# Optimization experiments

Measured on AMD Instinct MI355X. Metric: run time of the kernel, lower is better.

Reference implementation:

```python
import jax, jax.numpy as jnp
import numpy as np

B, S, H = 2, 2048, 1024
N, DK = 16, 64          # heads, key/value dim (N*DK == H)
DF = 4096               # FFN hidden
SCALE = 1.0 / float(DK) ** 0.5
EPS = 1e-5


def _layer_norm(x, g, b):
    mu = jnp.mean(x, axis=-1, keepdims=True)
    var = jnp.var(x, axis=-1, keepdims=True)
    return (x - mu) * jax.lax.rsqrt(var + EPS) * g + b


def setup_inputs() -> dict:
    key = jax.random.key(0)
    ks = jax.random.split(key, 12)
    s = 0.02
    return {
        "x": jax.random.normal(ks[0], (B, S, H), dtype=jnp.float32),
        "Wq": jax.random.normal(ks[1], (N * DK, H), dtype=jnp.float32) * s,
        "bq": jnp.zeros((N * DK,), jnp.float32),
        "Wk": jax.random.normal(ks[2], (N * DK, H), dtype=jnp.float32) * s,
        "bk": jnp.zeros((N * DK,), jnp.float32),
        "Wv": jax.random.normal(ks[3], (N * DK, H), dtype=jnp.float32) * s,
        "bv": jnp.zeros((N * DK,), jnp.float32),
        "Wo": jax.random.normal(ks[4], (H, N * DK), dtype=jnp.float32) * s,
        "bo": jnp.zeros((H,), jnp.float32),
        "W1": jax.random.normal(ks[5], (DF, H), dtype=jnp.float32) * s,
        "b1": jnp.zeros((DF,), jnp.float32),
        "W2": jax.random.normal(ks[6], (H, DF), dtype=jnp.float32) * s,
        "b2": jnp.zeros((H,), jnp.float32),
        "ln1_g": jnp.ones((H,), jnp.float32),
        "ln1_b": jnp.zeros((H,), jnp.float32),
        "ln2_g": jnp.ones((H,), jnp.float32),
        "ln2_b": jnp.zeros((H,), jnp.float32),
    }


def _mha(x, Wq, bq, Wk, bk, Wv, bv, Wo, bo):
    b = x.shape[0]
    q = (x @ Wq.T + bq).reshape(b, -1, N, DK)  # [B,T,N,DK]
    k = (x @ Wk.T + bk).reshape(b, -1, N, DK)
    v = (x @ Wv.T + bv).reshape(b, -1, N, DK)
    # naive full-score attention, faithful to torch einsum layout
    scores = jnp.einsum('btnd,bsnd->tsbn', q, k) * SCALE  # [T,S,B,N]
    p = jax.nn.softmax(scores, axis=1)                    # softmax over S (dim=1)
    attn = jnp.einsum('tsbn,bsnd->btnd', p, v)            # [B,T,N,DK]
    attn = attn.reshape(b, attn.shape[1], -1)             # [B,T,N*DK]
    return attn @ Wo.T + bo


def reference(x, Wq, bq, Wk, bk, Wv, bv, Wo, bo, W1, b1, W2, b2,
              ln1_g, ln1_b, ln2_g, ln2_b):
    # post-LN encoder layer: x = LN(x + MHA(x)); x = LN(x + FFN(x))
    h = _layer_norm(x + _mha(x, Wq, bq, Wk, bk, Wv, bv, Wo, bo), ln1_g, ln1_b)
    ff = jax.nn.relu(h @ W1.T + b1) @ W2.T + b2
    return _layer_norm(h + ff, ln2_g, ln2_b)
```

## Files before the change

### kernel.cpp

```cpp
#include <hip/hip_runtime.h>
#include <stdint.h>


typedef unsigned short u16;
typedef __bf16 bf16x8 __attribute__((ext_vector_type(8)));
typedef float  f32x4  __attribute__((ext_vector_type(4)));

__device__ __forceinline__ u16 f2bf(float f) {
    unsigned int u = __float_as_uint(f);
    u += 0x7FFFu + ((u >> 16) & 1u);
    return (u16)(u >> 16);
}

__device__ __forceinline__ float bf2f(u16 v) {
    return __uint_as_float((unsigned)v << 16);
}

__device__ __forceinline__ unsigned pack_bf16_hi(float lo, float hi) {
#if __has_builtin(__builtin_amdgcn_perm)
    return __builtin_amdgcn_perm(__float_as_uint(hi), __float_as_uint(lo), 0x07060302u);
#else
    return (__float_as_uint(lo) >> 16) | (__float_as_uint(hi) & 0xFFFF0000u);
#endif
}

__device__ __forceinline__ void async_load16(const u16* g, u16* l) {
    __builtin_amdgcn_global_load_lds(
        (__attribute__((address_space(1))) void*)g,
        (__attribute__((address_space(3))) void*)l, 16, 0, 0);
}

struct CvtArgs {
    const float* src[7];
    u16*         dst[7];
    int          n[7];
};

__global__ __launch_bounds__(256) void k_cvt_all(CvtArgs a) {
    const int seg = blockIdx.y;
    const int i = (blockIdx.x * 256 + threadIdx.x) * 8;
    if (i >= a.n[seg]) return;
    const float* in = a.src[seg];
    u16* out = a.dst[seg];
    float4 x = *(const float4*)(in + i);
    float4 y = *(const float4*)(in + i + 4);
    uint4 o;
    o.x = (unsigned)f2bf(x.x) | ((unsigned)f2bf(x.y) << 16);
    o.y = (unsigned)f2bf(x.z) | ((unsigned)f2bf(x.w) << 16);
    o.z = (unsigned)f2bf(y.x) | ((unsigned)f2bf(y.y) << 16);
    o.w = (unsigned)f2bf(y.z) | ((unsigned)f2bf(y.w) << 16);
    *(uint4*)(out + i) = o;
}

__global__ __launch_bounds__(256) void k_concat3(const float* __restrict__ a,
                                                 const float* __restrict__ b,
                                                 const float* __restrict__ c,
                                                 float* __restrict__ out) {
    int i = blockIdx.x * 256 + threadIdx.x;
    if (i >= 3072) return;
    out[i] = (i < 1024) ? a[i] : (i < 2048 ? b[i - 1024] : c[i - 2048]);
}

template<int OUT_BF16, int RELU>
__global__ __launch_bounds__(512, 2) void k_gemm256(
    const u16* __restrict__ A, const u16* __restrict__ Bw,
    const float* __restrict__ bias, void* __restrict__ Y,
    int M, int N, int K)
{
    __shared__ u16 As[2][256 * 64];
    __shared__ u16 Bs[2][256 * 64];
    const int tid  = threadIdx.x;
    const int wave = tid >> 6, lane = tid & 63;
    const int lm = lane & 15, lq = lane >> 4;
    const int wr = wave >> 2;
    const int wc = wave & 3;
    const int m0 = blockIdx.x * 256, n0 = blockIdx.y * 256;
    const int ksz = K / gridDim.z;
    const int ks  = blockIdx.z * ksz;
    const int NT  = ksz >> 6;

    size_t goffA[4], goffB[4];
#pragma unroll
    for (int i = 0; i < 4; i++) {
        const int c = i * 512 + tid;
        const int row = c >> 3, kcp = c & 7;
        const int kcl = kcp ^ (row & 7);
        goffA[i] = (size_t)(m0 + row) * K + kcl * 8;
        goffB[i] = (size_t)(n0 + row) * K + kcl * 8;
    }

    const int ach0 = ((0 + lq) ^ (lm & 7)) * 8;
    const int ach1 = ((4 + lq) ^ (lm & 7)) * 8;
    const int albase = (wr * 128 + lm) * 64;
    const int blbase = (wc * 64 + lm) * 64;

    f32x4 acc[8][4];
#pragma unroll
    for (int i = 0; i < 8; i++)
#pragma unroll
        for (int j = 0; j < 4; j++) acc[i][j] = (f32x4){0.f, 0.f, 0.f, 0.f};

#define STAGE256(T, p)                                                          \
    {                                                                           \
        const int k0_ = ks + (T) * 64;                                          \
        _Pragma("unroll")                                                       \
        for (int i_ = 0; i_ < 4; i_++) {                                        \
            async_load16(A  + goffA[i_] + k0_,                                  \
                         &As[p][(i_ * 512 + wave * 64) * 8]);                   \
            async_load16(Bw + goffB[i_] + k0_,                                  \
                         &Bs[p][(i_ * 512 + wave * 64) * 8]);                   \
        }                                                                       \
    }

#define LOADQ(dst, q)                                                           \
    {                                                                           \
        _Pragma("unroll")                                                       \
        for (int ii_ = 0; ii_ < 2; ii_++) {                                     \
            dst[ii_][0] = *(const bf16x8*)(Ab + albase + ((q)*2 + ii_) * 1024 + ach0); \
            dst[ii_][1] = *(const bf16x8*)(Ab + albase + ((q)*2 + ii_) * 1024 + ach1); \
        }                                                                       \
    }

#define MFMAQ(src, q)                                                           \
    {                                                                           \
        _Pragma("unroll")                                                       \
        for (int ii_ = 0; ii_ < 2; ii_++)                                       \
            _Pragma("unroll")                                                   \
            for (int j_ = 0; j_ < 4; j_++) {                                    \
                acc[(q)*2 + ii_][j_] = __builtin_amdgcn_mfma_f32_16x16x32_bf16( \
                    src[ii_][0], bfr[0][j_], acc[(q)*2 + ii_][j_], 0, 0, 0);    \
                acc[(q)*2 + ii_][j_] = __builtin_amdgcn_mfma_f32_16x16x32_bf16( \
                    src[ii_][1], bfr[1][j_], acc[(q)*2 + ii_][j_], 0, 0, 0);    \
            }                                                                   \
    }

    STAGE256(0, 0);
    STAGE256(1, 1);
    asm volatile("s_waitcnt vmcnt(8)" ::: "memory");
    __builtin_amdgcn_s_barrier();
    __builtin_amdgcn_sched_barrier(0);

    for (int T = 0; T < NT; ++T) {
        const int p = T & 1;
        const u16* Ab = As[p];
        const u16* Bb = Bs[p];

        bf16x8 bfr[2][4];
#pragma unroll
        for (int j = 0; j < 4; j++) {
            bfr[0][j] = *(const bf16x8*)(Bb + blbase + j * 1024 + ach0);
            bfr[1][j] = *(const bf16x8*)(Bb + blbase + j * 1024 + ach1);
        }
        bf16x8 aA[2][2], aB[2][2];
        LOADQ(aA, 0);
        LOADQ(aB, 1);
        MFMAQ(aA, 0);
        LOADQ(aA, 2);
        MFMAQ(aB, 1);
        LOADQ(aB, 3);
        MFMAQ(aA, 2);
        MFMAQ(aB, 3);

        __builtin_amdgcn_sched_barrier(0);
        __builtin_amdgcn_s_barrier();
        __builtin_amdgcn_sched_barrier(0);

        if (T + 2 < NT) {
            STAGE256(T + 2, p);
            asm volatile("s_waitcnt vmcnt(8)" ::: "memory");
            __builtin_amdgcn_s_barrier();
            __builtin_amdgcn_sched_barrier(0);
        } else if (T + 1 < NT) {
            asm volatile("s_waitcnt vmcnt(0)" ::: "memory");
            __builtin_amdgcn_s_barrier();
            __builtin_amdgcn_sched_barrier(0);
        }
    }
#undef STAGE256
#undef LOADQ
#undef MFMAQ

    const float bsc = (blockIdx.z == 0) ? 1.f : 0.f;
    const size_t zoff = (size_t)blockIdx.z * M * N;
#pragma unroll
    for (int i = 0; i < 8; i++) {
        const int mg = m0 + wr * 128 + i * 16 + lq * 4;
#pragma unroll
        for (int j = 0; j < 4; j++) {
            const int ng = n0 + wc * 64 + j * 16 + lm;
            const float bv = bias[ng] * bsc;
#pragma unroll
            for (int r = 0; r < 4; r++) {
                float v = acc[i][j][r] + bv;
                if (RELU) v = fmaxf(v, 0.f);
                if (OUT_BF16) ((u16*)Y)[zoff + (size_t)(mg + r) * N + ng] = f2bf(v);
                else          ((float*)Y)[zoff + (size_t)(mg + r) * N + ng] = v;
            }
        }
    }
}

template<int OUT_BF16, int RELU>
__global__ __launch_bounds__(256, 4) void k_gemm_bt(
    const u16* __restrict__ A, const u16* __restrict__ Bw,
    const float* __restrict__ bias, void* __restrict__ Y,
    int M, int N, int K)
{
    __shared__ u16 As[128 * 64];
    __shared__ u16 Bs[128 * 64];
    const int tid  = threadIdx.x;
    const int wave = tid >> 6, lane = tid & 63;
    const int lm = lane & 15, lq = lane >> 4;
    const int m0 = blockIdx.x * 128, n0 = blockIdx.y * 128;
    const int wr = (wave >> 1) * 64, wc = (wave & 1) * 64;

    const int ksz = K / gridDim.z;
    const int ks  = blockIdx.z * ksz, ke = ks + ksz;

    const int sr8 = wave * 8 + (lane >> 3);
    const int scx = ((lane & 7) * 8) ^ (((sr8 >> 2) & 3) << 4);
    const size_t arow = (size_t)(m0 + sr8) * K + scx;
    const size_t brow = (size_t)(n0 + sr8) * K + scx;
    const int sw = ((lm >> 2) & 3) << 4;

    f32x4 acc[4][4];
#pragma unroll
    for (int i = 0; i < 4; i++)
#pragma unroll
        for (int j = 0; j < 4; j++) acc[i][j] = (f32x4){0.f, 0.f, 0.f, 0.f};

    for (int k0 = ks; k0 < ke; k0 += 64) {
        __syncthreads();
#pragma unroll
        for (int j = 0; j < 4; j++) {
            async_load16(A  + arow + (size_t)(j * 32) * K + k0, As + j * 2048 + wave * 512);
            async_load16(Bw + brow + (size_t)(j * 32) * K + k0, Bs + j * 2048 + wave * 512);
        }
        __syncthreads();

#pragma unroll
        for (int h = 0; h < 2; h++) {
            const int cofs = (h * 32 + lq * 8) ^ sw;
            bf16x8 af[4], bf[4];
#pragma unroll
            for (int i = 0; i < 4; i++)
                af[i] = *(const bf16x8*)(As + (wr + i * 16 + lm) * 64 + cofs);
#pragma unroll
            for (int j = 0; j < 4; j++)
                bf[j] = *(const bf16x8*)(Bs + (wc + j * 16 + lm) * 64 + cofs);
#pragma unroll
            for (int i = 0; i < 4; i++)
#pragma unroll
                for (int j = 0; j < 4; j++)
                    acc[i][j] = __builtin_amdgcn_mfma_f32_16x16x32_bf16(af[i], bf[j], acc[i][j], 0, 0, 0);
        }
    }

    const float bsc = (blockIdx.z == 0) ? 1.f : 0.f;
    const size_t zoff = (size_t)blockIdx.z * M * N;
#pragma unroll
    for (int i = 0; i < 4; i++) {
        const int mg = m0 + wr + i * 16 + lq * 4;
#pragma unroll
        for (int j = 0; j < 4; j++) {
            const int ng = n0 + wc + j * 16 + lm;
            const float bv = bias[ng] * bsc;
#pragma unroll
            for (int r = 0; r < 4; r++) {
                float v = acc[i][j][r] + bv;
                if (RELU) v = fmaxf(v, 0.f);
                if (OUT_BF16) ((u16*)Y)[zoff + (size_t)(mg + r) * N + ng] = f2bf(v);
                else          ((float*)Y)[zoff + (size_t)(mg + r) * N + ng] = v;
            }
        }
    }
}

__global__ __launch_bounds__(256) void k_transpose_v(const u16* __restrict__ qkv,
                                                     u16* __restrict__ vt) {
    __shared__ u16 T[64 * 72];
    const int tid = threadIdx.x;
    const int t0 = blockIdx.x * 64;
    const int bn = blockIdx.y;
    const int b = bn >> 4, n = bn & 15;
    {
        const int r = tid >> 2, c = (tid & 3) * 16;
        const u16* src = qkv + (size_t)(b * 2048 + t0 + r) * 3072 + 2048 + n * 64 + c;
        *(uint4*)&T[r * 72 + c]     = *(const uint4*)(src);
        *(uint4*)&T[r * 72 + c + 8] = *(const uint4*)(src + 8);
    }
    __syncthreads();
    {
        const int d = tid >> 2, c = (tid & 3) * 16;
        union { u16 h[16]; uint4 v[2]; } tmp;
#pragma unroll
        for (int j = 0; j < 16; j++) {
            const int w = c + j;
            const int k = ((w & 3) << 4) + (w >> 2);
            tmp.h[j] = T[k * 72 + d];
        }
        u16* dst = vt + (size_t)(bn * 64 + d) * 2048 + t0 + c;
        *(uint4*)(dst)     = tmp.v[0];
        *(uint4*)(dst + 8) = tmp.v[1];
    }
}

__global__ __launch_bounds__(256, 2) void k_flash(const u16* __restrict__ qkv,
                                                  const u16* __restrict__ vt,
                                                  u16* __restrict__ attn) {
    __shared__ u16 Ks[2][64 * 72];
    __shared__ u16 Vs[2][64 * 72];
    __shared__ u16 Ps[4 * 32 * 72];
    const int tid = threadIdx.x, wave = tid >> 6, lane = tid & 63;
    const int lm = lane & 15, lq = lane >> 4;
    const int b = blockIdx.z, n = blockIdx.y, qt0 = blockIdx.x * 128;

    bf16x8 qf[2][2];
#pragma unroll
    for (int mh = 0; mh < 2; mh++) {
        const u16* qp = qkv + (size_t)(b * 2048 + qt0 + wave * 32 + mh * 16 + lm) * 3072
                        + n * 64 + lq * 8;
        const bf16x8 q0r = *(const bf16x8*)(qp);
        const bf16x8 q1r = *(const bf16x8*)(qp + 32);
#pragma unroll
        for (int j = 0; j < 8; j++) {
            qf[mh][0][j] = (__bf16)((float)q0r[j] * 0.18033688f);
            qf[mh][1][j] = (__bf16)((float)q1r[j] * 0.18033688f);
        }
    }

    float lsum[2][4];
    f32x4 oacc[2][4];
#pragma unroll
    for (int mh = 0; mh < 2; mh++)
#pragma unroll
        for (int r = 0; r < 4; r++) { lsum[mh][r] = 0.f; }
#pragma unroll
    for (int mh = 0; mh < 2; mh++)
#pragma unroll
        for (int dt = 0; dt < 4; dt++) oacc[mh][dt] = (f32x4){0.f, 0.f, 0.f, 0.f};

    const int sr = tid >> 2, sc = (tid & 3) * 16;
    const u16* kg = qkv + (size_t)(b * 2048 + sr) * 3072 + 1024 + n * 64 + sc;
    const u16* vg = vt + (size_t)((b * 16 + n) * 64 + sr) * 2048 + sc;
    u16* PsW = Ps + wave * 32 * 72;

    {
        uint4 a0 = *(const uint4*)(kg);
        uint4 a1 = *(const uint4*)(kg + 8);
        uint4 b0 = *(const uint4*)(vg);
        uint4 b1 = *(const uint4*)(vg + 8);
        *(uint4*)&Ks[0][sr * 72 + sc]     = a0;
        *(uint4*)&Ks[0][sr * 72 + sc + 8] = a1;
        *(uint4*)&Vs[0][sr * 72 + sc]     = b0;
        *(uint4*)&Vs[0][sr * 72 + sc + 8] = b1;
    }
    uint4 kr0 = *(const uint4*)(kg + 3072);
    uint4 kr1 = *(const uint4*)(kg + 3072 + 8);
    uint4 vr0 = *(const uint4*)(vg + 64);
    uint4 vr1 = *(const uint4*)(vg + 64 + 8);
    __syncthreads();

    int c = 0;
    for (int kt = 0; kt < 2048; kt += 64) {
        if (kt + 64 < 2048) {
            u16* Kd = Ks[c ^ 1];
            u16* Vd = Vs[c ^ 1];
            *(uint4*)&Kd[sr * 72 + sc]     = kr0;
            *(uint4*)&Kd[sr * 72 + sc + 8] = kr1;
            *(uint4*)&Vd[sr * 72 + sc]     = vr0;
            *(uint4*)&Vd[sr * 72 + sc + 8] = vr1;
            if (kt + 128 < 2048) {
                kr0 = *(const uint4*)(kg + (size_t)(kt + 128) * 3072);
                kr1 = *(const uint4*)(kg + (size_t)(kt + 128) * 3072 + 8);
                vr0 = *(const uint4*)(vg + kt + 128);
                vr1 = *(const uint4*)(vg + kt + 128 + 8);
            }
        }

        const u16* Kc = Ks[c];
        const u16* Vc = Vs[c];

        f32x4 sf[2][4];
        __builtin_amdgcn_s_setprio(1);
#pragma unroll
        for (int nt = 0; nt < 4; nt++) {
            const bf16x8 kf0 = *(const bf16x8*)(Kc + (nt * 16 + lm) * 72 + lq * 8);
            const bf16x8 kf1 = *(const bf16x8*)(Kc + (nt * 16 + lm) * 72 + lq * 8 + 32);
#pragma unroll
            for (int mh = 0; mh < 2; mh++) {
                f32x4 z = (f32x4){0.f, 0.f, 0.f, 0.f};
                z = __builtin_amdgcn_mfma_f32_16x16x32_bf16(qf[mh][0], kf0, z, 0, 0, 0);
                z = __builtin_amdgcn_mfma_f32_16x16x32_bf16(qf[mh][1], kf1, z, 0, 0, 0);
                sf[mh][nt] = z;
            }
        }
        __builtin_amdgcn_s_setprio(0);

#pragma unroll
        for (int mh = 0; mh < 2; mh++)
#pragma unroll
            for (int r = 0; r < 4; r++) {
                const float p0 = __builtin_amdgcn_exp2f(sf[mh][0][r]);
                const float p1 = __builtin_amdgcn_exp2f(sf[mh][1][r]);
                const float p2 = __builtin_amdgcn_exp2f(sf[mh][2][r]);
                const float p3 = __builtin_amdgcn_exp2f(sf[mh][3][r]);
                lsum[mh][r] += (p0 + p1) + (p2 + p3);
                uint2 w;
                w.x = pack_bf16_hi(p0, p1);
                w.y = pack_bf16_hi(p2, p3);
                *(uint2*)&PsW[(mh * 16 + lq * 4 + r) * 72 + lm * 4] = w;
            }

        __builtin_amdgcn_s_setprio(1);
#pragma unroll
        for (int s2 = 0; s2 < 2; s2++) {
            bf16x8 pf[2];
#pragma unroll
            for (int mh = 0; mh < 2; mh++)
                pf[mh] = *(const bf16x8*)(PsW + (mh * 16 + lm) * 72 + s2 * 32 + lq * 8);
#pragma unroll
            for (int dt = 0; dt < 4; dt++) {
                const bf16x8 vf = *(const bf16x8*)(Vc + (dt * 16 + lm) * 72 + s2 * 32 + lq * 8);
#pragma unroll
                for (int mh = 0; mh < 2; mh++)
                    oacc[mh][dt] = __builtin_amdgcn_mfma_f32_16x16x32_bf16(pf[mh], vf, oacc[mh][dt], 0, 0, 0);
            }
        }
        __builtin_amdgcn_s_setprio(0);

        __syncthreads();
        c ^= 1;
    }

#pragma unroll
    for (int mh = 0; mh < 2; mh++)
#pragma unroll
        for (int r = 0; r < 4; r++) {
#pragma unroll
            for (int off = 8; off >= 1; off >>= 1)
                lsum[mh][r] += __shfl_xor(lsum[mh][r], off, 16);
            lsum[mh][r] = 1.f / lsum[mh][r];
        }
#pragma unroll
    for (int mh = 0; mh < 2; mh++)
#pragma unroll
        for (int dt = 0; dt < 4; dt++)
#pragma unroll
            for (int r = 0; r < 4; r++) {
                const float o = oacc[mh][dt][r] * lsum[mh][r];
                attn[(size_t)(b * 2048 + qt0 + wave * 32 + mh * 16 + lq * 4 + r) * 1024
                     + n * 64 + dt * 16 + lm] = f2bf(o);
            }
}

template<int WRITE_BF16>
__global__ __launch_bounds__(256) void k_ln_p4(const float* __restrict__ a,
                                               const u16* __restrict__ pb,
                                               const float* __restrict__ g,
                                               const float* __restrict__ be,
                                               float* __restrict__ outf,
                                               u16* __restrict__ outb) {
    const int row = blockIdx.x, tid = threadIdx.x;
    const size_t base = (size_t)row * 1024 + tid * 4;
    const float4 av = *(const float4*)(a + base);
    float x0 = av.x, x1 = av.y, x2 = av.z, x3 = av.w;
#pragma unroll
    for (int z = 0; z < 4; z++) {
        const uint2 w = *(const uint2*)(pb + (size_t)z * 4096 * 1024 + base);
        x0 += __uint_as_float(w.x << 16);
        x1 += __uint_as_float(w.x & 0xFFFF0000u);
        x2 += __uint_as_float(w.y << 16);
        x3 += __uint_as_float(w.y & 0xFFFF0000u);
    }
    float s1 = x0 + x1 + x2 + x3;
    float s2 = x0 * x0 + x1 * x1 + x2 * x2 + x3 * x3;
#pragma unroll
    for (int off = 32; off >= 1; off >>= 1) {
        s1 += __shfl_down(s1, off);
        s2 += __shfl_down(s2, off);
    }
    __shared__ float red[8];
    __shared__ float stats[2];
    const int wave = tid >> 6, lane = tid & 63;
    if (lane == 0) { red[wave] = s1; red[4 + wave] = s2; }
    __syncthreads();
    if (tid == 0) {
        const float t1 = red[0] + red[1] + red[2] + red[3];
        const float t2 = red[4] + red[5] + red[6] + red[7];
        const float mean = t1 * (1.f / 1024.f);
        const float var = t2 * (1.f / 1024.f) - mean * mean;
        stats[0] = mean;
        stats[1] = rsqrtf(var + 1e-5f);
    }
    __syncthreads();
    const float mean = stats[0], rstd = stats[1];
    const int c = tid * 4;
    const float4 gv = *(const float4*)(g + c);
    const float4 bev = *(const float4*)(be + c);
    float4 y;
    y.x = (x0 - mean) * rstd * gv.x + bev.x;
    y.y = (x1 - mean) * rstd * gv.y + bev.y;
    y.z = (x2 - mean) * rstd * gv.z + bev.z;
    y.w = (x3 - mean) * rstd * gv.w + bev.w;
    *(float4*)(outf + base) = y;
    if (WRITE_BF16) {
        uint2 o;
        o.x = (unsigned)f2bf(y.x) | ((unsigned)f2bf(y.y) << 16);
        o.y = (unsigned)f2bf(y.z) | ((unsigned)f2bf(y.w) << 16);
        *(uint2*)(outb + base) = o;
    }
}

extern "C" void kernel_launch(void* const* d_in, const int* in_sizes, int n_in,
                              void* d_out, int out_size, void* d_ws, size_t ws_size,
                              hipStream_t stream) {
    const float* x   = (const float*)d_in[0];
    const float* Wq  = (const float*)d_in[1];
    const float* bq  = (const float*)d_in[2];
    const float* Wk  = (const float*)d_in[3];
    const float* bk  = (const float*)d_in[4];
    const float* Wv  = (const float*)d_in[5];
    const float* bv  = (const float*)d_in[6];
    const float* Wo  = (const float*)d_in[7];
    const float* bo  = (const float*)d_in[8];
    const float* W1  = (const float*)d_in[9];
    const float* b1  = (const float*)d_in[10];
    const float* W2  = (const float*)d_in[11];
    const float* b2  = (const float*)d_in[12];
    const float* g1  = (const float*)d_in[13];
    const float* be1 = (const float*)d_in[14];
    const float* g2  = (const float*)d_in[15];
    const float* be2 = (const float*)d_in[16];

    char* ws = (char*)d_ws;
    const size_t MB = 1024 * 1024;
    u16*   wqkv = (u16*)(ws + 0);
    u16*   wo_b = (u16*)(ws + 6 * MB);
    u16*   w1_b = (u16*)(ws + 8 * MB);
    u16*   w2_b = (u16*)(ws + 16 * MB);
    float* bqkv = (float*)(ws + 24 * MB);
    u16*   xb   = (u16*)(ws + 25 * MB);
    u16*   qkv  = (u16*)(ws + 33 * MB);
    u16*   vt   = (u16*)(ws + 57 * MB);
    u16*   attn = (u16*)(ws + 65 * MB);
    u16*   op4  = (u16*)(ws + 33 * MB);
    float* h    = (float*)(ws + 65 * MB);
    u16*   hb   = (u16*)(ws + 81 * MB);
    u16*   ff1  = (u16*)(ws + 33 * MB);
    u16*   fp4  = (u16*)(ws + 81 * MB);

    CvtArgs ca;
    ca.src[0] = x;  ca.dst[0] = xb;                  ca.n[0] = 4096 * 1024;
    ca.src[1] = Wq; ca.dst[1] = wqkv;                ca.n[1] = 1024 * 1024;
    ca.src[2] = Wk; ca.dst[2] = wqkv + 1024 * 1024;  ca.n[2] = 1024 * 1024;
    ca.src[3] = Wv; ca.dst[3] = wqkv + 2 * 1024 * 1024; ca.n[3] = 1024 * 1024;
    ca.src[4] = Wo; ca.dst[4] = wo_b;                ca.n[4] = 1024 * 1024;
    ca.src[5] = W1; ca.dst[5] = w1_b;                ca.n[5] = 4096 * 1024;
    ca.src[6] = W2; ca.dst[6] = w2_b;                ca.n[6] = 4096 * 1024;
    k_cvt_all<<<dim3(2048, 7), 256, 0, stream>>>(ca);
    k_concat3<<<12, 256, 0, stream>>>(bq, bk, bv, bqkv);

    k_gemm256<1, 0><<<dim3(16, 12), 512, 0, stream>>>(
        xb, wqkv, bqkv, qkv, 4096, 3072, 1024);

    k_transpose_v<<<dim3(32, 32), 256, 0, stream>>>(qkv, vt);

    k_flash<<<dim3(16, 16, 2), 256, 0, stream>>>(qkv, vt, attn);

    k_gemm_bt<1, 0><<<dim3(32, 8, 4), 256, 0, stream>>>(
        attn, wo_b, bo, op4, 4096, 1024, 1024);

    k_ln_p4<1><<<4096, 256, 0, stream>>>(x, op4, g1, be1, h, hb);

    k_gemm256<1, 1><<<dim3(16, 16), 512, 0, stream>>>(
        hb, w1_b, b1, ff1, 4096, 4096, 1024);

    k_gemm256<1, 0><<<dim3(16, 4, 4), 512, 0, stream>>>(
        ff1, w2_b, b2, fp4, 4096, 1024, 4096);

    k_ln_p4<0><<<4096, 256, 0, stream>>>(h, fp4, g2, be2, (float*)d_out, nullptr);
}
```

Measured before the change: 332.0 us.

## Restructure 256x256 GEMM into eight-phase pipeline with split A/B prefetch

Reworks the main loop of the large bf16 GEMM into four sub-phases per K-tile. Each phase issues a half-tile global prefetch: A for the next tile into the other buffer, and B two tiles ahead into the current buffer after its fragments are in registers. Barriers and lgkmcnt waits interleave the LDS reads with MFMA bursts, and s_setprio raises wave priority during the MFMAs. The aim is to overlap global loads with compute more finely and reduce stalls from the per-tile barrier. In exchange there are more barriers per tile and a more fragile buffer-hazard ordering.

```diff
diff --git a/kernel.cpp b/kernel.cpp
--- a/kernel.cpp
+++ b/kernel.cpp
@@ -62,7 +62,7 @@
 }
 
 template<int OUT_BF16, int RELU>
-__global__ __launch_bounds__(512, 2) void k_gemm256(
+__global__ __launch_bounds__(512, 2) void k_gemm8p(
     const u16* __restrict__ A, const u16* __restrict__ Bw,
     const float* __restrict__ bias, void* __restrict__ Y,
     int M, int N, int K)
@@ -72,27 +72,27 @@
     const int tid  = threadIdx.x;
     const int wave = tid >> 6, lane = tid & 63;
     const int lm = lane & 15, lq = lane >> 4;
-    const int wr = wave >> 2;
-    const int wc = wave & 3;
+    const int wr = wave >> 2, wc = wave & 3;
     const int m0 = blockIdx.x * 256, n0 = blockIdx.y * 256;
     const int ksz = K / gridDim.z;
     const int ks  = blockIdx.z * ksz;
     const int NT  = ksz >> 6;
 
-    size_t goffA[4], goffB[4];
-#pragma unroll
-    for (int i = 0; i < 4; i++) {
-        const int c = i * 512 + tid;
-        const int row = c >> 3, kcp = c & 7;
-        const int kcl = kcp ^ (row & 7);
-        goffA[i] = (size_t)(m0 + row) * K + kcl * 8;
-        goffB[i] = (size_t)(n0 + row) * K + kcl * 8;
-    }
+    size_t gA[2], gB[2];
+#pragma unroll
+    for (int j = 0; j < 2; j++) {
+        const int c = j * 512 + tid;
+        const int rl = c >> 3, kcp = c & 7;
+        const int kcl = kcp ^ (rl & 7);
+        gA[j] = (size_t)(m0 + rl) * K + kcl * 8;
+        gB[j] = (size_t)(n0 + rl) * K + kcl * 8;
+    }
+    const size_t hstep = (size_t)128 * K;
 
     const int ach0 = ((0 + lq) ^ (lm & 7)) * 8;
     const int ach1 = ((4 + lq) ^ (lm & 7)) * 8;
-    const int albase = (wr * 128 + lm) * 64;
-    const int blbase = (wc * 64 + lm) * 64;
+    const int abase = (wr * 128 + lm) * 64;
+    const int bbase = (wc * 64 + lm) * 64;
 
     f32x4 acc[8][4];
 #pragma unroll
@@ -100,43 +100,31 @@
 #pragma unroll
         for (int j = 0; j < 4; j++) acc[i][j] = (f32x4){0.f, 0.f, 0.f, 0.f};
 
-#define STAGE256(T, p)                                                          \
+#define STAGE_A(T, p, h)                                                        \
     {                                                                           \
-        const int k0_ = ks + (T) * 64;                                          \
+        const size_t k0_ = (size_t)ks + (size_t)(T) * 64;                       \
         _Pragma("unroll")                                                       \
-        for (int i_ = 0; i_ < 4; i_++) {                                        \
-            async_load16(A  + goffA[i_] + k0_,                                  \
-                         &As[p][(i_ * 512 + wave * 64) * 8]);                   \
-            async_load16(Bw + goffB[i_] + k0_,                                  \
-                         &Bs[p][(i_ * 512 + wave * 64) * 8]);                   \
-        }                                                                       \
-    }
-
-#define LOADQ(dst, q)                                                           \
+        for (int j_ = 0; j_ < 2; j_++)                                          \
+            async_load16(A + gA[j_] + (size_t)(h) * hstep + k0_,                \
+                         &As[p][((h) * 1024 + j_ * 512 + wave * 64) * 8]);      \
+    }
+#define STAGE_B(T, p, h)                                                        \
     {                                                                           \
+        const size_t k0_ = (size_t)ks + (size_t)(T) * 64;                       \
         _Pragma("unroll")                                                       \
-        for (int ii_ = 0; ii_ < 2; ii_++) {                                     \
-            dst[ii_][0] = *(const bf16x8*)(Ab + albase + ((q)*2 + ii_) * 1024 + ach0); \
-            dst[ii_][1] = *(const bf16x8*)(Ab + albase + ((q)*2 + ii_) * 1024 + ach1); \
-        }                                                                       \
-    }
-
-#define MFMAQ(src, q)                                                           \
-    {                                                                           \
-        _Pragma("unroll")                                                       \
-        for (int ii_ = 0; ii_ < 2; ii_++)                                       \
-            _Pragma("unroll")                                                   \
-            for (int j_ = 0; j_ < 4; j_++) {                                    \
-                acc[(q)*2 + ii_][j_] = __builtin_amdgcn_mfma_f32_16x16x32_bf16( \
-                    src[ii_][0], bfr[0][j_], acc[(q)*2 + ii_][j_], 0, 0, 0);    \
-                acc[(q)*2 + ii_][j_] = __builtin_amdgcn_mfma_f32_16x16x32_bf16( \
-                    src[ii_][1], bfr[1][j_], acc[(q)*2 + ii_][j_], 0, 0, 0);    \
-            }                                                                   \
-    }
-
-    STAGE256(0, 0);
-    STAGE256(1, 1);
-    asm volatile("s_waitcnt vmcnt(8)" ::: "memory");
+        for (int j_ = 0; j_ < 2; j_++)                                          \
+            async_load16(Bw + gB[j_] + (size_t)(h) * hstep + k0_,               \
+                         &Bs[p][((h) * 1024 + j_ * 512 + wave * 64) * 8]);      \
+    }
+
+    STAGE_A(0, 0, 0); STAGE_A(0, 0, 1);
+    STAGE_B(0, 0, 0); STAGE_B(0, 0, 1);
+    if (NT > 1) {
+        STAGE_B(1, 1, 0); STAGE_B(1, 1, 1);
+        asm volatile("s_waitcnt vmcnt(4)" ::: "memory");
+    } else {
+        asm volatile("s_waitcnt vmcnt(0)" ::: "memory");
+    }
     __builtin_amdgcn_s_barrier();
     __builtin_amdgcn_sched_barrier(0);
 
@@ -144,41 +132,117 @@
         const int p = T & 1;
         const u16* Ab = As[p];
         const u16* Bb = Bs[p];
-
-        bf16x8 bfr[2][4];
-#pragma unroll
-        for (int j = 0; j < 4; j++) {
-            bfr[0][j] = *(const bf16x8*)(Bb + blbase + j * 1024 + ach0);
-            bfr[1][j] = *(const bf16x8*)(Bb + blbase + j * 1024 + ach1);
-        }
-        bf16x8 aA[2][2], aB[2][2];
-        LOADQ(aA, 0);
-        LOADQ(aB, 1);
-        MFMAQ(aA, 0);
-        LOADQ(aA, 2);
-        MFMAQ(aB, 1);
-        LOADQ(aB, 3);
-        MFMAQ(aA, 2);
-        MFMAQ(aB, 3);
-
-        __builtin_amdgcn_sched_barrier(0);
-        __builtin_amdgcn_s_barrier();
-        __builtin_amdgcn_sched_barrier(0);
-
-        if (T + 2 < NT) {
-            STAGE256(T + 2, p);
-            asm volatile("s_waitcnt vmcnt(8)" ::: "memory");
-            __builtin_amdgcn_s_barrier();
-            __builtin_amdgcn_sched_barrier(0);
-        } else if (T + 1 < NT) {
-            asm volatile("s_waitcnt vmcnt(0)" ::: "memory");
-            __builtin_amdgcn_s_barrier();
-            __builtin_amdgcn_sched_barrier(0);
-        }
-    }
-#undef STAGE256
-#undef LOADQ
-#undef MFMAQ
+        bf16x8 bF[4][2];
+
+        {
+#pragma unroll
+            for (int n = 0; n < 4; n++) {
+                bF[n][0] = *(const bf16x8*)(Bb + bbase + n * 1024 + ach0);
+                bF[n][1] = *(const bf16x8*)(Bb + bbase + n * 1024 + ach1);
+            }
+            bf16x8 aF[2][2];
+#pragma unroll
+            for (int i = 0; i < 2; i++) {
+                aF[i][0] = *(const bf16x8*)(Ab + abase + (0 + i) * 1024 + ach0);
+                aF[i][1] = *(const bf16x8*)(Ab + abase + (0 + i) * 1024 + ach1);
+            }
+            if (T + 1 < NT) STAGE_A(T + 1, p ^ 1, 0);
+            __builtin_amdgcn_sched_barrier(0);
+            __builtin_amdgcn_s_barrier();
+            asm volatile("s_waitcnt lgkmcnt(0)" ::: "memory");
+            __builtin_amdgcn_sched_barrier(0);
+            __builtin_amdgcn_s_setprio(1);
+#pragma unroll
+            for (int i = 0; i < 2; i++)
+#pragma unroll
+                for (int n = 0; n < 4; n++) {
+                    acc[0 + i][n] = __builtin_amdgcn_mfma_f32_16x16x32_bf16(aF[i][0], bF[n][0], acc[0 + i][n], 0, 0, 0);
+                    acc[0 + i][n] = __builtin_amdgcn_mfma_f32_16x16x32_bf16(aF[i][1], bF[n][1], acc[0 + i][n], 0, 0, 0);
+                }
+            __builtin_amdgcn_s_setprio(0);
+            __builtin_amdgcn_sched_barrier(0);
+            __builtin_amdgcn_s_barrier();
+        }
+        {
+            bf16x8 aF[2][2];
+#pragma unroll
+            for (int i = 0; i < 2; i++) {
+                aF[i][0] = *(const bf16x8*)(Ab + abase + (2 + i) * 1024 + ach0);
+                aF[i][1] = *(const bf16x8*)(Ab + abase + (2 + i) * 1024 + ach1);
+            }
+            if (T + 1 < NT) STAGE_A(T + 1, p ^ 1, 1);
+            __builtin_amdgcn_sched_barrier(0);
+            __builtin_amdgcn_s_barrier();
+            asm volatile("s_waitcnt lgkmcnt(0)" ::: "memory");
+            __builtin_amdgcn_sched_barrier(0);
+            __builtin_amdgcn_s_setprio(1);
+#pragma unroll
+            for (int i = 0; i < 2; i++)
+#pragma unroll
+                for (int n = 0; n < 4; n++) {
+                    acc[2 + i][n] = __builtin_amdgcn_mfma_f32_16x16x32_bf16(aF[i][0], bF[n][0], acc[2 + i][n], 0, 0, 0);
+                    acc[2 + i][n] = __builtin_amdgcn_mfma_f32_16x16x32_bf16(aF[i][1], bF[n][1], acc[2 + i][n], 0, 0, 0);
+                }
+            __builtin_amdgcn_s_setprio(0);
+            __builtin_amdgcn_sched_barrier(0);
+            __builtin_amdgcn_s_barrier();
+        }
+        {
+            bf16x8 aF[2][2];
+#pragma unroll
+            for (int i = 0; i < 2; i++) {
+                aF[i][0] = *(const bf16x8*)(Ab + abase + (4 + i) * 1024 + ach0);
+                aF[i][1] = *(const bf16x8*)(Ab + abase + (4 + i) * 1024 + ach1);
+            }
+            if (T + 2 < NT) STAGE_B(T + 2, p, 0);
+            __builtin_amdgcn_sched_barrier(0);
+            __builtin_amdgcn_s_barrier();
+            asm volatile("s_waitcnt lgkmcnt(0)" ::: "memory");
+            __builtin_amdgcn_sched_barrier(0);
+            __builtin_amdgcn_s_setprio(1);
+#pragma unroll
+            for (int i = 0; i < 2; i++)
+#pragma unroll
+                for (int n = 0; n < 4; n++) {
+                    acc[4 + i][n] = __builtin_amdgcn_mfma_f32_16x16x32_bf16(aF[i][0], bF[n][0], acc[4 + i][n], 0, 0, 0);
+                    acc[4 + i][n] = __builtin_amdgcn_mfma_f32_16x16x32_bf16(aF[i][1], bF[n][1], acc[4 + i][n], 0, 0, 0);
+                }
+            __builtin_amdgcn_s_setprio(0);
+            __builtin_amdgcn_sched_barrier(0);
+            __builtin_amdgcn_s_barrier();
+        }
+        {
+            bf16x8 aF[2][2];
+#pragma unroll
+            for (int i = 0; i < 2; i++) {
+                aF[i][0] = *(const bf16x8*)(Ab + abase + (6 + i) * 1024 + ach0);
+                aF[i][1] = *(const bf16x8*)(Ab + abase + (6 + i) * 1024 + ach1);
+            }
+            if (T + 2 < NT) STAGE_B(T + 2, p, 1);
+            __builtin_amdgcn_sched_barrier(0);
+            __builtin_amdgcn_s_barrier();
+            asm volatile("s_waitcnt lgkmcnt(0)" ::: "memory");
+            __builtin_amdgcn_sched_barrier(0);
+            __builtin_amdgcn_s_setprio(1);
+#pragma unroll
+            for (int i = 0; i < 2; i++)
+#pragma unroll
+                for (int n = 0; n < 4; n++) {
+                    acc[6 + i][n] = __builtin_amdgcn_mfma_f32_16x16x32_bf16(aF[i][0], bF[n][0], acc[6 + i][n], 0, 0, 0);
+                    acc[6 + i][n] = __builtin_amdgcn_mfma_f32_16x16x32_bf16(aF[i][1], bF[n][1], acc[6 + i][n], 0, 0, 0);
+                }
+            __builtin_amdgcn_s_setprio(0);
+            __builtin_amdgcn_sched_barrier(0);
+            if (T + 2 < NT) {
+                asm volatile("s_waitcnt vmcnt(4)" ::: "memory");
+            } else if (T + 1 < NT) {
+                asm volatile("s_waitcnt vmcnt(0)" ::: "memory");
+            }
+            __builtin_amdgcn_s_barrier();
+        }
+    }
+#undef STAGE_A
+#undef STAGE_B
 
     const float bsc = (blockIdx.z == 0) ? 1.f : 0.f;
     const size_t zoff = (size_t)blockIdx.z * M * N;
@@ -561,7 +625,7 @@
     k_cvt_all<<<dim3(2048, 7), 256, 0, stream>>>(ca);
     k_concat3<<<12, 256, 0, stream>>>(bq, bk, bv, bqkv);
 
-    k_gemm256<1, 0><<<dim3(16, 12), 512, 0, stream>>>(
+    k_gemm8p<1, 0><<<dim3(16, 12), 512, 0, stream>>>(
         xb, wqkv, bqkv, qkv, 4096, 3072, 1024);
 
     k_transpose_v<<<dim3(32, 32), 256, 0, stream>>>(qkv, vt);
@@ -573,10 +637,10 @@
 
     k_ln_p4<1><<<4096, 256, 0, stream>>>(x, op4, g1, be1, h, hb);
 
-    k_gemm256<1, 1><<<dim3(16, 16), 512, 0, stream>>>(
+    k_gemm8p<1, 1><<<dim3(16, 16), 512, 0, stream>>>(
         hb, w1_b, b1, ff1, 4096, 4096, 1024);
 
-    k_gemm256<1, 0><<<dim3(16, 4, 4), 512, 0, stream>>>(
+    k_gemm8p<1, 0><<<dim3(16, 4, 4), 512, 0, stream>>>(
         ff1, w2_b, b2, fp4, 4096, 1024, 4096);
 
     k_ln_p4<0><<<4096, 256, 0, stream>>>(h, fp4, g2, be2, (float*)d_out, nullptr);
```

New measurement: 353.4 us. 6.4% more time.
